# Optimization experiments

Measured on AMD Instinct MI355X. Metric: run time of the kernel, lower is better.

## Reference

```python
import jax, jax.numpy as jnp
import numpy as np

N = 100000   # nodes
E = 3200000  # edges (avg degree 32)
D_IN = 128
C = 64
EPS = 1e-5  # GraphNorm eps (PyG default)


def _graph_norm(x, alpha, gamma, beta):
    # GraphNorm over a single graph: all N nodes form one segment.
    mean = jnp.mean(x, axis=0, keepdims=True)            # [1, C]
    xc = x - alpha * mean                                # learnable mean-scale
    var = jnp.mean(xc * xc, axis=0, keepdims=True)       # [1, C]
    return gamma * xc * jax.lax.rsqrt(var + EPS) + beta


def _gcn_conv(x, W, bias, src, dst, dinv):
    # GCN with implicit self-loops: out = D^-1/2 (A+I) D^-1/2 (x W) + b
    xw = x @ W                                           # [N, C]
    coef = (dinv[src] * dinv[dst])[:, None]              # [E, 1]
    msg = xw[src] * coef                                 # [E, C] gather
    agg = jax.ops.segment_sum(msg, dst, num_segments=N)  # [N, C] scatter
    agg = agg + xw * (dinv * dinv)[:, None]              # self-loop term
    return agg + bias


def setup_inputs() -> dict:
    key = jax.random.key(0)
    ks = jax.random.split(key, 4)
    x = jax.random.normal(ks[0], (N, D_IN), dtype=jnp.float32)
    edge_index = jax.random.randint(ks[1], (2, E), 0, N, dtype=jnp.int64)
    W0 = jax.random.normal(ks[2], (D_IN, C), dtype=jnp.float32) * (1.0 / np.sqrt(D_IN))
    Ws = jax.random.normal(ks[3], (2, C, C), dtype=jnp.float32) * (1.0 / np.sqrt(C))
    b = jnp.zeros((3, C), dtype=jnp.float32)
    alpha = jnp.ones((3, C), dtype=jnp.float32)
    gamma = jnp.ones((3, C), dtype=jnp.float32)
    beta = jnp.zeros((3, C), dtype=jnp.float32)
    return {"x": x, "edge_index": edge_index, "W0": W0, "Ws": Ws,
            "b": b, "alpha": alpha, "gamma": gamma, "beta": beta}


def reference(x, edge_index, W0, Ws, b, alpha, gamma, beta):
    src, dst = edge_index[0], edge_index[1]
    deg = 1.0 + jax.ops.segment_sum(jnp.ones((E,), dtype=x.dtype), dst, num_segments=N)
    dinv = jax.lax.rsqrt(deg)                            # [N]
    h = _gcn_conv(x, W0, b[0], src, dst, dinv)
    h = _graph_norm(h, alpha[0], gamma[0], beta[0])      # dropout = identity (eval)
    for i in range(2):
        h = _gcn_conv(h, Ws[i], b[i + 1], src, dst, dinv)
        h = _graph_norm(h, alpha[i + 1], gamma[i + 1], beta[i + 1])
    return h
```

## Files before the change

### kernel.cpp

```cpp
#include <hip/hip_runtime.h>
#include <hip/hip_bf16.h>


#define EPS 1e-5f

typedef __attribute__((ext_vector_type(8))) short bf16x8;
typedef __attribute__((ext_vector_type(4))) float f32x4;

__device__ __forceinline__ float bf_lo(unsigned u) {
    union { unsigned u; float f; } c; c.u = u << 16; return c.f;
}
__device__ __forceinline__ float bf_hi(unsigned u) {
    union { unsigned u; float f; } c; c.u = u & 0xffff0000u; return c.f;
}
__device__ __forceinline__ unsigned pack_bf2(float a, float b) {
    union { __hip_bfloat16 h; unsigned short u; } ca, cb;
    ca.h = __float2bfloat16(a);
    cb.h = __float2bfloat16(b);
    return (unsigned)ca.u | ((unsigned)cb.u << 16);
}
__device__ __forceinline__ short bfb(float f) {
    union { __hip_bfloat16 h; short s; } u; u.h = __float2bfloat16(f); return u.s;
}

__global__ __launch_bounds__(256) void k_hist(const int* __restrict__ dst, int* __restrict__ hist,
                                              int E, int SEG, int NBKT) {
    __shared__ int h[2048];
    int t = threadIdx.x;
    for (int b = t; b < NBKT; b += 256) h[b] = 0;
    __syncthreads();
    int i0 = blockIdx.x * SEG, i1 = min(E, i0 + SEG);
    for (int i = i0 + t * 4; i < i1; i += 1024) {
        if (i + 3 < i1) {
            int4 d = *(const int4*)(dst + i);
            atomicAdd(&h[d.x >> 6], 1);
            atomicAdd(&h[d.y >> 6], 1);
            atomicAdd(&h[d.z >> 6], 1);
            atomicAdd(&h[d.w >> 6], 1);
        } else {
            for (int q = i; q < i1; ++q) atomicAdd(&h[dst[q] >> 6], 1);
        }
    }
    __syncthreads();
    for (int b = t; b < NBKT; b += 256) hist[blockIdx.x * NBKT + b] = h[b];
}

__global__ __launch_bounds__(256) void k_scanA(const int* __restrict__ hist, int* __restrict__ chunkScan,
                                               int* __restrict__ chunkTot, int NBKT, int SCAN_N) {
    __shared__ int ls[256];
    int t = threadIdx.x;
    int base = blockIdx.x * 1024 + t * 4;
    int v[4];
#pragma unroll
    for (int j = 0; j < 4; ++j) {
        int l = base + j;
        v[j] = 0;
        if (l < SCAN_N) {
            int blk = l & 255, bkt = l >> 8;
            v[j] = hist[blk * NBKT + bkt];
        }
    }
    int s = v[0] + v[1] + v[2] + v[3];
    ls[t] = s;
    __syncthreads();
    for (int off = 1; off < 256; off <<= 1) {
        int val = (t >= off) ? ls[t - off] : 0;
        __syncthreads();
        ls[t] += val;
        __syncthreads();
    }
    int run = ls[t] - s;
#pragma unroll
    for (int j = 0; j < 4; ++j) {
        chunkScan[base + j] = run;
        run += v[j];
    }
    if (t == 255) chunkTot[blockIdx.x] = ls[255];
}

__global__ void k_scanB(const int* __restrict__ chunkTot, int* __restrict__ chunkBase, int NCH) {
    __shared__ int s[512];
    int t = threadIdx.x;
    s[t] = (t < NCH) ? chunkTot[t] : 0;
    s[t + 256] = (t + 256 < NCH) ? chunkTot[t + 256] : 0;
    __syncthreads();
    for (int off = 1; off < 512; off <<= 1) {
        int a0 = (t >= off) ? s[t - off] : 0;
        int a1 = (t + 256 >= off) ? s[t + 256 - off] : 0;
        __syncthreads();
        s[t] += a0;
        s[t + 256] += a1;
        __syncthreads();
    }
    if (t < NCH) chunkBase[t] = t ? s[t - 1] : 0;
    if (t + 256 < NCH) chunkBase[t + 256] = s[t + 255];
}

__global__ __launch_bounds__(256) void k_scatter_part(const int* __restrict__ src, const int* __restrict__ dst,
                                                      const int* __restrict__ chunkScan,
                                                      const int* __restrict__ chunkBase,
                                                      int* __restrict__ packed, int E, int SEG, int NBKT) {
    __shared__ int cur[2048];
    int blk = blockIdx.x, t = threadIdx.x;
    for (int b = t; b < NBKT; b += 256) {
        int l = b * 256 + blk;
        cur[b] = chunkScan[l] + chunkBase[l >> 10];
    }
    __syncthreads();
    int i0 = blk * SEG, i1 = min(E, i0 + SEG);
    for (int i = i0 + t * 4; i < i1; i += 1024) {
        if (i + 3 < i1) {
            int4 d = *(const int4*)(dst + i);
            int4 s = *(const int4*)(src + i);
            int p;
            p = atomicAdd(&cur[d.x >> 6], 1); packed[p] = (int)(((unsigned)(d.x & 63) << 26) | (unsigned)s.x);
            p = atomicAdd(&cur[d.y >> 6], 1); packed[p] = (int)(((unsigned)(d.y & 63) << 26) | (unsigned)s.y);
            p = atomicAdd(&cur[d.z >> 6], 1); packed[p] = (int)(((unsigned)(d.z & 63) << 26) | (unsigned)s.z);
            p = atomicAdd(&cur[d.w >> 6], 1); packed[p] = (int)(((unsigned)(d.w & 63) << 26) | (unsigned)s.w);
        } else {
            for (int q = i; q < i1; ++q) {
                int dd = dst[q];
                int p = atomicAdd(&cur[dd >> 6], 1);
                packed[p] = (int)(((unsigned)(dd & 63) << 26) | (unsigned)src[q]);
            }
        }
    }
}

__global__ __launch_bounds__(256) void k_ellfill(const int* __restrict__ packed,
                                                 const int* __restrict__ chunkScan,
                                                 const int* __restrict__ chunkBase,
                                                 int* __restrict__ ell, int* __restrict__ cursor,
                                                 float* __restrict__ dinv,
                                                 int CAP, int NBKT, int N, int E) {
    __shared__ int ellLoc[64 * 96];
    __shared__ int cnt[64];
    int bkt = blockIdx.x, t = threadIdx.x;
    if (t < 64) cnt[t] = 0;
    __syncthreads();
    int l0 = bkt * 256;
    int bs = chunkScan[l0] + chunkBase[l0 >> 10];
    int be = E;
    if (bkt + 1 < NBKT) {
        int l1 = (bkt + 1) * 256;
        be = chunkScan[l1] + chunkBase[l1 >> 10];
    }
    for (int i = bs + t; i < be; i += 256) {
        unsigned p = (unsigned)packed[i];
        int s = (int)(p & 0x03FFFFFFu);
        int ld = (int)(p >> 26);
        int slot = atomicAdd(&cnt[ld], 1);
        if (slot < CAP) ellLoc[ld * CAP + slot] = s;
    }
    __syncthreads();
    int lo = bkt << 6;
    int total = 64 * CAP;
    for (int idx = t; idx < total; idx += 256) {
        int ld = idx / CAP;
        int s = idx - ld * CAP;
        if (lo + ld < N && s < min(cnt[ld], CAP))
            ell[(size_t)lo * CAP + idx] = ellLoc[idx];
    }
    if (t < 64 && lo + t < N) {
        int dg = min(cnt[t], CAP);
        cursor[lo + t] = (lo + t) * CAP + dg;
        dinv[lo + t] = rsqrtf(1.0f + (float)cnt[t]);
    }
}

__global__ __launch_bounds__(256) void k_cursor_init(int* cursor, int CAP, int n) {
    int i = blockIdx.x * 256 + threadIdx.x;
    if (i < n) cursor[i] = i * CAP;
}

__global__ __launch_bounds__(256) void k_fill_ell(const int* __restrict__ src, const int* __restrict__ dst,
                                                  int* cursor, int* __restrict__ ell, int E,
                                                  int lo, int hi) {
    int i = (blockIdx.x * 256 + threadIdx.x) * 4;
    if (i + 3 < E) {
        int4 d = *(const int4*)(dst + i);
        int4 s = *(const int4*)(src + i);
        if (d.x >= lo && d.x < hi) ell[atomicAdd(&cursor[d.x], 1)] = s.x;
        if (d.y >= lo && d.y < hi) ell[atomicAdd(&cursor[d.y], 1)] = s.y;
        if (d.z >= lo && d.z < hi) ell[atomicAdd(&cursor[d.z], 1)] = s.z;
        if (d.w >= lo && d.w < hi) ell[atomicAdd(&cursor[d.w], 1)] = s.w;
    } else {
        for (int t = i; t < E; ++t) {
            int d = dst[t];
            if (d >= lo && d < hi) ell[atomicAdd(&cursor[d], 1)] = src[t];
        }
    }
}

__global__ __launch_bounds__(256) void k_deg_dinv(const int* __restrict__ cursor, float* dinv, int CAP, int n) {
    int i = blockIdx.x * 256 + threadIdx.x;
    if (i < n) dinv[i] = rsqrtf(1.0f + (float)(cursor[i] - i * CAP));
}

template <int K, bool AFP32>
__global__ __launch_bounds__(256) void gemm_mfma(const void* __restrict__ in_,
                                                 const unsigned short* __restrict__ Wb,
                                                 const float* __restrict__ bbv,
                                                 const float* __restrict__ dinv,
                                                 __hip_bfloat16* __restrict__ out, int N) {
    constexpr int NC = K / 32;
    int tid = threadIdx.x;
    int lane = tid & 63, w = tid >> 6;
    int r0 = blockIdx.x * 64;
    int col = w * 16 + (lane & 15);
    int kg = lane >> 4;

    bf16x8 bfrag[NC];
#pragma unroll
    for (int kc = 0; kc < NC; ++kc)
        bfrag[kc] = *(const bf16x8*)(Wb + (size_t)col * K + kc * 32 + kg * 8);
    float bbc = bbv ? bbv[col] : 0.f;

#pragma unroll 1
    for (int rt = 0; rt < 4; ++rt) {
        int arow = r0 + rt * 16 + (lane & 15);
        int arow_c = min(arow, N - 1);
        f32x4 acc = {0.f, 0.f, 0.f, 0.f};
#pragma unroll
        for (int kc = 0; kc < NC; ++kc) {
            bf16x8 afrag;
            if (AFP32) {
                const float* in = (const float*)in_ + (size_t)arow_c * K + kc * 32 + kg * 8;
                float4 lo = *(const float4*)in;
                float4 hi = *(const float4*)(in + 4);
                union { short s[8]; bf16x8 v; } cv;
                cv.s[0] = bfb(lo.x); cv.s[1] = bfb(lo.y); cv.s[2] = bfb(lo.z); cv.s[3] = bfb(lo.w);
                cv.s[4] = bfb(hi.x); cv.s[5] = bfb(hi.y); cv.s[6] = bfb(hi.z); cv.s[7] = bfb(hi.w);
                afrag = cv.v;
            } else {
                const unsigned short* in = (const unsigned short*)in_;
                afrag = *(const bf16x8*)(in + (size_t)arow_c * K + kc * 32 + kg * 8);
            }
            acc = __builtin_amdgcn_mfma_f32_16x16x32_bf16(afrag, bfrag[kc], acc, 0, 0, 0);
        }
#pragma unroll
        for (int j = 0; j < 4; ++j) {
            int row = r0 + rt * 16 + kg * 4 + j;
            if (row < N)
                out[(size_t)row * 64 + col] = __float2bfloat16((acc[j] + bbc) * dinv[row]);
        }
    }
}

__global__ void k_packW0(const float* __restrict__ W0, unsigned short* __restrict__ Wb) {
    int c = threadIdx.x;
    for (int k = 0; k < 128; ++k) Wb[c * 128 + k] = (unsigned short)bfb(W0[k * 64 + c]);
}

template <bool OUT_BF16>
__global__ __launch_bounds__(256, 4) void k_pull(const int* __restrict__ cursor,
                                                 const int* __restrict__ ell,
                                                 const float* __restrict__ dinv,
                                                 const uint4* __restrict__ xwh,
                                                 const float* __restrict__ bias,
                                                 float* __restrict__ aggf,
                                                 __hip_bfloat16* __restrict__ aggh,
                                                 float* __restrict__ sums, float* __restrict__ sumsq,
                                                 int CAP, int N) {
    int tid = threadIdx.x;
    int lane = tid & 63;
    int g = lane >> 3;
    int cl = lane & 7;
    float bs[8];
#pragma unroll
    for (int k = 0; k < 8; ++k) bs[k] = bias[cl * 8 + k];
    float s_acc[8] = {0, 0, 0, 0, 0, 0, 0, 0};
    float q_acc[8] = {0, 0, 0, 0, 0, 0, 0, 0};

    int slot = (blockIdx.x * 4 + (tid >> 6)) * 8 + g;
    int nslots = gridDim.x * 32;
    for (int n = slot; n < N; n += nslots) {
        int beg = n * CAP, end = cursor[n];
        int last = end - 1;
        float acc[8];
        {
            uint4 v = xwh[(size_t)n * 8 + cl];
            acc[0] = bf_lo(v.x); acc[1] = bf_hi(v.x);
            acc[2] = bf_lo(v.y); acc[3] = bf_hi(v.y);
            acc[4] = bf_lo(v.z); acc[5] = bf_hi(v.z);
            acc[6] = bf_lo(v.w); acc[7] = bf_hi(v.w);
        }
        int i = beg;
        for (; i + 8 <= end; i += 8) {
            int4 ia = *(const int4*)&ell[i];
            int4 ib = *(const int4*)&ell[i + 4];
            uint4 vv[8];
            vv[0] = xwh[(size_t)ia.x * 8 + cl];
            vv[1] = xwh[(size_t)ia.y * 8 + cl];
            vv[2] = xwh[(size_t)ia.z * 8 + cl];
            vv[3] = xwh[(size_t)ia.w * 8 + cl];
            vv[4] = xwh[(size_t)ib.x * 8 + cl];
            vv[5] = xwh[(size_t)ib.y * 8 + cl];
            vv[6] = xwh[(size_t)ib.z * 8 + cl];
            vv[7] = xwh[(size_t)ib.w * 8 + cl];
#pragma unroll
            for (int k = 0; k < 8; ++k) {
                acc[0] += bf_lo(vv[k].x); acc[1] += bf_hi(vv[k].x);
                acc[2] += bf_lo(vv[k].y); acc[3] += bf_hi(vv[k].y);
                acc[4] += bf_lo(vv[k].z); acc[5] += bf_hi(vv[k].z);
                acc[6] += bf_lo(vv[k].w); acc[7] += bf_hi(vv[k].w);
            }
        }
        if (i < end) {
            int4 ia = *(const int4*)&ell[i];
            int4 ib = *(const int4*)&ell[i + 4];
            int ss[8];
            ss[0] = ia.x; ss[1] = ia.y; ss[2] = ia.z; ss[3] = ia.w;
            ss[4] = ib.x; ss[5] = ib.y; ss[6] = ib.z; ss[7] = ib.w;
#pragma unroll
            for (int k = 0; k < 8; ++k) ss[k] = (i + k <= last) ? ss[k] : 0;
            uint4 vv[8];
#pragma unroll
            for (int k = 0; k < 8; ++k) vv[k] = xwh[(size_t)ss[k] * 8 + cl];
#pragma unroll
            for (int k = 0; k < 8; ++k) {
                if (i + k > last) { vv[k].x = 0; vv[k].y = 0; vv[k].z = 0; vv[k].w = 0; }
                acc[0] += bf_lo(vv[k].x); acc[1] += bf_hi(vv[k].x);
                acc[2] += bf_lo(vv[k].y); acc[3] += bf_hi(vv[k].y);
                acc[4] += bf_lo(vv[k].z); acc[5] += bf_hi(vv[k].z);
                acc[6] += bf_lo(vv[k].w); acc[7] += bf_hi(vv[k].w);
            }
        }
        float dn = dinv[n];
        float r[8];
#pragma unroll
        for (int k = 0; k < 8; ++k) {
            r[k] = dn * acc[k] + bs[k];
            s_acc[k] += r[k];
            q_acc[k] += r[k] * r[k];
        }
        if (OUT_BF16) {
            uint4 o;
            o.x = pack_bf2(r[0], r[1]);
            o.y = pack_bf2(r[2], r[3]);
            o.z = pack_bf2(r[4], r[5]);
            o.w = pack_bf2(r[6], r[7]);
            *(uint4*)((unsigned short*)aggh + (size_t)n * 64 + cl * 8) = o;
        } else {
            float4* d4 = (float4*)(aggf + (size_t)n * 64 + cl * 8);
            d4[0] = make_float4(r[0], r[1], r[2], r[3]);
            d4[1] = make_float4(r[4], r[5], r[6], r[7]);
        }
    }

    __shared__ float lsum[256][9], lsq[256][9];
#pragma unroll
    for (int k = 0; k < 8; ++k) { lsum[tid][k] = s_acc[k]; lsq[tid][k] = q_acc[k]; }
    __syncthreads();
    if (tid < 64) {
        int cl_t = tid >> 3, k_t = tid & 7;
        float s = 0.f, q = 0.f;
        for (int j = 0; j < 32; ++j) {
            int l = cl_t + 8 * j;
            s += lsum[l][k_t];
            q += lsq[l][k_t];
        }
        atomicAdd(&sums[tid], s);
        atomicAdd(&sumsq[tid], q);
    }
}

__global__ void k_params2(float* __restrict__ sums, float* __restrict__ sumsq,
                          const float* __restrict__ alpha, const float* __restrict__ gamma,
                          const float* __restrict__ beta, const float* __restrict__ W,
                          float* __restrict__ scale, float* __restrict__ shift,
                          unsigned short* __restrict__ Wb, float* __restrict__ bb, int N) {
    __shared__ float ssc[64], ssh[64];
    int c = threadIdx.x;
    float invN = 1.0f / (float)N;
    float m = sums[c] * invN;
    float ex2 = sumsq[c] * invN;
    float a = alpha[c];
    float var = ex2 - 2.0f * a * m * m + a * a * m * m;
    float sc = gamma[c] * rsqrtf(var + EPS);
    float sh = beta[c] - sc * a * m;
    scale[c] = sc;
    shift[c] = sh;
    ssc[c] = sc;
    ssh[c] = sh;
    sums[c] = 0.f;
    sumsq[c] = 0.f;
    __syncthreads();
    if (W) {
        float acc = 0.f;
        for (int k = 0; k < 64; ++k) {
            float w = W[k * 64 + c];
            Wb[c * 64 + k] = (unsigned short)bfb(ssc[k] * w);
            acc += ssh[k] * w;
        }
        bb[c] = acc;
    }
}

__global__ __launch_bounds__(256) void k_final(float* __restrict__ out, const float* __restrict__ scale,
                                               const float* __restrict__ shift, int n64) {
    int i = blockIdx.x * 256 + threadIdx.x;
    if (i < n64) out[i] = scale[i & 63] * out[i] + shift[i & 63];
}

extern "C" void kernel_launch(void* const* d_in, const int* in_sizes, int n_in,
                              void* d_out, int out_size, void* d_ws, size_t ws_size,
                              hipStream_t stream) {
    const float* x     = (const float*)d_in[0];
    const int*   ei    = (const int*)d_in[1];
    const float* W0    = (const float*)d_in[2];
    const float* Wsp   = (const float*)d_in[3];
    const float* b     = (const float*)d_in[4];
    const float* alpha = (const float*)d_in[5];
    const float* gamma = (const float*)d_in[6];
    const float* beta  = (const float*)d_in[7];

    const int N = in_sizes[0] / 128;
    const int E = in_sizes[1] / 2;
    const int* src = ei;
    const int* dst = ei + E;

    float* aggf = (float*)d_out;

    const int Na = ((N + 63) / 64) * 64;
    float* ws = (float*)d_ws;
    size_t off = 0;
    float* dinv  = ws + off; off += Na;
    __hip_bfloat16* xwh = (__hip_bfloat16*)(ws + off); off += (size_t)Na * 32;
    __hip_bfloat16* hb  = (__hip_bfloat16*)(ws + off); off += (size_t)Na * 32;
    float* sums  = ws + off; off += 64;
    float* sumsq = ws + off; off += 64;
    float* scbuf = ws + off; off += 64;
    float* shbuf = ws + off; off += 64;
    unsigned short* Wb = (unsigned short*)(ws + off); off += 4096;
    float* bbv   = ws + off; off += 64;
    int* cursor  = (int*)(ws + off); off += Na;

    int CAP = 96;
    while (CAP > 72 && (off + (size_t)N * CAP + 8) * 4 > ws_size) CAP -= 8;
    int* ell = (int*)(ws + off); off += (size_t)N * CAP + 8;

    const int n64 = N * 64;
    const int RB = (N + 63) / 64;
    const int NB = (N + 255) / 256;
    const int PB = (N + 63) / 64;

    const int NBKT = (N + 63) >> 6;
    const int NSEG = 256;
    int SEG = ((E + NSEG - 1) / NSEG + 3) & ~3;
    const int SCAN_N = NBKT * 256;
    const int NCH = (SCAN_N + 1023) / 1024;
    int* packed    = (int*)xwh;
    int* hist      = (int*)hb;
    int* chunkScan = hist + (size_t)NSEG * NBKT;
    int* chunkTot  = chunkScan + (size_t)NCH * 1024;
    int* chunkBase = chunkTot + NCH;
    bool fast_build = (NBKT <= 2048) && (NCH <= 512) && (N < (1 << 26)) &&
                      ((size_t)E <= (size_t)Na * 32) &&
                      ((size_t)NSEG * NBKT + (size_t)NCH * 1024 + 2 * NCH <= (size_t)Na * 32);

    if (fast_build) {
        k_hist<<<NSEG, 256, 0, stream>>>(dst, hist, E, SEG, NBKT);
        k_scanA<<<NCH, 256, 0, stream>>>(hist, chunkScan, chunkTot, NBKT, SCAN_N);
        k_scanB<<<1, 256, 0, stream>>>(chunkTot, chunkBase, NCH);
        k_scatter_part<<<NSEG, 256, 0, stream>>>(src, dst, chunkScan, chunkBase, packed, E, SEG, NBKT);
        k_ellfill<<<NBKT, 256, 0, stream>>>(packed, chunkScan, chunkBase, ell, cursor, dinv,
                                            CAP, NBKT, N, E);
    } else {
        k_cursor_init<<<NB, 256, 0, stream>>>(cursor, CAP, N);
        const int NCHUNK = 10;
        int cs = (N + NCHUNK - 1) / NCHUNK;
        const int EB4 = (E / 4 + 255) / 256;
        for (int c = 0; c < NCHUNK; ++c) {
            int lo = c * cs, hi = min(N, lo + cs);
            k_fill_ell<<<EB4, 256, 0, stream>>>(src, dst, cursor, ell, E, lo, hi);
        }
        k_deg_dinv<<<NB, 256, 0, stream>>>(cursor, dinv, CAP, N);
    }

    hipMemsetAsync(sums, 0, 128 * sizeof(float), stream);
    k_packW0<<<1, 64, 0, stream>>>(W0, Wb);

    for (int layer = 0; layer < 3; ++layer) {
        if (layer == 0) {
            gemm_mfma<128, true><<<RB, 256, 0, stream>>>(x, Wb, nullptr, dinv, xwh, N);
        } else {
            gemm_mfma<64, false><<<RB, 256, 0, stream>>>(hb, Wb, bbv, dinv, xwh, N);
        }
        if (layer < 2) {
            k_pull<true><<<PB, 256, 0, stream>>>(cursor, ell, dinv, (const uint4*)xwh,
                                                 b + layer * 64, nullptr, hb,
                                                 sums, sumsq, CAP, N);
        } else {
            k_pull<false><<<PB, 256, 0, stream>>>(cursor, ell, dinv, (const uint4*)xwh,
                                                  b + layer * 64, aggf, nullptr,
                                                  sums, sumsq, CAP, N);
        }
        const float* Wnext = (layer < 2) ? (Wsp + (size_t)layer * 64 * 64) : nullptr;
        k_params2<<<1, 64, 0, stream>>>(sums, sumsq, alpha + layer * 64, gamma + layer * 64,
                                        beta + layer * 64, Wnext, scbuf, shbuf, Wb, bbv, N);
    }
    k_final<<<(n64 + 255) / 256, 256, 0, stream>>>(aggf, scbuf, shbuf, n64);
}
```

Measured before the change: 386.3 us.

## Split feature tables into four 16-channel planes and pull each plane separately

The GEMM now writes its bf16 output as four planar 16-column slabs of 32 bytes per row instead of one 128-byte row. The pull kernel makes four passes, one per slab, gathering 4 bytes per lane from a table four times smaller, so the gathered working set is more likely to stay in cache. The cost is four passes over the ELL index list and cursors, narrower gathers of 32 bytes per neighbor, and more passes' worth of loop overhead.

```diff
diff --git a/kernel.cpp b/kernel.cpp
--- a/kernel.cpp
+++ b/kernel.cpp
@@ -202,7 +202,8 @@
                                                  const unsigned short* __restrict__ Wb,
                                                  const float* __restrict__ bbv,
                                                  const float* __restrict__ dinv,
-                                                 __hip_bfloat16* __restrict__ out, int N) {
+                                                 unsigned short* __restrict__ out16,
+                                                 int N) {
     constexpr int NC = K / 32;
     int tid = threadIdx.x;
     int lane = tid & 63, w = tid >> 6;
@@ -234,7 +235,8 @@
                 afrag = cv.v;
             } else {
                 const unsigned short* in = (const unsigned short*)in_;
-                afrag = *(const bf16x8*)(in + (size_t)arow_c * K + kc * 32 + kg * 8);
+                int pa = kc * 2 + (kg >> 1);
+                afrag = *(const bf16x8*)(in + ((size_t)pa * N + arow_c) * 16 + (kg & 1) * 8);
             }
             acc = __builtin_amdgcn_mfma_f32_16x16x32_bf16(afrag, bfrag[kc], acc, 0, 0, 0);
         }
@@ -242,7 +244,8 @@
         for (int j = 0; j < 4; ++j) {
             int row = r0 + rt * 16 + kg * 4 + j;
             if (row < N)
-                out[(size_t)row * 64 + col] = __float2bfloat16((acc[j] + bbc) * dinv[row]);
+                out16[((size_t)w * N + row) * 16 + (lane & 15)] =
+                    (unsigned short)bfb((acc[j] + bbc) * dinv[row]);
         }
     }
 }
@@ -256,109 +259,90 @@
 __global__ __launch_bounds__(256, 4) void k_pull(const int* __restrict__ cursor,
                                                  const int* __restrict__ ell,
                                                  const float* __restrict__ dinv,
-                                                 const uint4* __restrict__ xwh,
+                                                 const unsigned* __restrict__ xws8,
                                                  const float* __restrict__ bias,
                                                  float* __restrict__ aggf,
-                                                 __hip_bfloat16* __restrict__ aggh,
+                                                 unsigned* __restrict__ aggh8,
                                                  float* __restrict__ sums, float* __restrict__ sumsq,
                                                  int CAP, int N) {
     int tid = threadIdx.x;
     int lane = tid & 63;
     int g = lane >> 3;
     int cl = lane & 7;
-    float bs[8];
-#pragma unroll
-    for (int k = 0; k < 8; ++k) bs[k] = bias[cl * 8 + k];
-    float s_acc[8] = {0, 0, 0, 0, 0, 0, 0, 0};
-    float q_acc[8] = {0, 0, 0, 0, 0, 0, 0, 0};
-
-    int slot = (blockIdx.x * 4 + (tid >> 6)) * 8 + g;
+    __shared__ float lsum[256][9], lsq[256][9];
+
+    int slot0 = (blockIdx.x * 4 + (tid >> 6)) * 8 + g;
     int nslots = gridDim.x * 32;
-    for (int n = slot; n < N; n += nslots) {
-        int beg = n * CAP, end = cursor[n];
-        int last = end - 1;
-        float acc[8];
-        {
-            uint4 v = xwh[(size_t)n * 8 + cl];
-            acc[0] = bf_lo(v.x); acc[1] = bf_hi(v.x);
-            acc[2] = bf_lo(v.y); acc[3] = bf_hi(v.y);
-            acc[4] = bf_lo(v.z); acc[5] = bf_hi(v.z);
-            acc[6] = bf_lo(v.w); acc[7] = bf_hi(v.w);
-        }
-        int i = beg;
-        for (; i + 8 <= end; i += 8) {
-            int4 ia = *(const int4*)&ell[i];
-            int4 ib = *(const int4*)&ell[i + 4];
-            uint4 vv[8];
-            vv[0] = xwh[(size_t)ia.x * 8 + cl];
-            vv[1] = xwh[(size_t)ia.y * 8 + cl];
-            vv[2] = xwh[(size_t)ia.z * 8 + cl];
-            vv[3] = xwh[(size_t)ia.w * 8 + cl];
-            vv[4] = xwh[(size_t)ib.x * 8 + cl];
-            vv[5] = xwh[(size_t)ib.y * 8 + cl];
-            vv[6] = xwh[(size_t)ib.z * 8 + cl];
-            vv[7] = xwh[(size_t)ib.w * 8 + cl];
-#pragma unroll
-            for (int k = 0; k < 8; ++k) {
-                acc[0] += bf_lo(vv[k].x); acc[1] += bf_hi(vv[k].x);
-                acc[2] += bf_lo(vv[k].y); acc[3] += bf_hi(vv[k].y);
-                acc[4] += bf_lo(vv[k].z); acc[5] += bf_hi(vv[k].z);
-                acc[6] += bf_lo(vv[k].w); acc[7] += bf_hi(vv[k].w);
+
+#pragma unroll 1
+    for (int p = 0; p < 4; ++p) {
+        const unsigned* tab = xws8 + (size_t)p * N * 8;
+        float bs0 = bias[p * 16 + cl * 2];
+        float bs1 = bias[p * 16 + cl * 2 + 1];
+        float sp0 = 0.f, sp1 = 0.f, qp0 = 0.f, qp1 = 0.f;
+        for (int n = slot0; n < N; n += nslots) {
+            int beg = n * CAP, end = cursor[n];
+            int last = end - 1;
+            unsigned su = tab[(size_t)n * 8 + cl];
+            float a0 = bf_lo(su), a1 = bf_hi(su);
+            int i = beg;
+            for (; i + 8 <= end; i += 8) {
+                int4 ia = *(const int4*)&ell[i];
+                int4 ib = *(const int4*)&ell[i + 4];
+                unsigned v0 = tab[(size_t)ia.x * 8 + cl];
+                unsigned v1 = tab[(size_t)ia.y * 8 + cl];
+                unsigned v2 = tab[(size_t)ia.z * 8 + cl];
+                unsigned v3 = tab[(size_t)ia.w * 8 + cl];
+                unsigned v4 = tab[(size_t)ib.x * 8 + cl];
+                unsigned v5 = tab[(size_t)ib.y * 8 + cl];
+                unsigned v6 = tab[(size_t)ib.z * 8 + cl];
+                unsigned v7 = tab[(size_t)ib.w * 8 + cl];
+                a0 += bf_lo(v0) + bf_lo(v1) + bf_lo(v2) + bf_lo(v3)
+                    + bf_lo(v4) + bf_lo(v5) + bf_lo(v6) + bf_lo(v7);
+                a1 += bf_hi(v0) + bf_hi(v1) + bf_hi(v2) + bf_hi(v3)
+                    + bf_hi(v4) + bf_hi(v5) + bf_hi(v6) + bf_hi(v7);
             }
-        }
-        if (i < end) {
-            int4 ia = *(const int4*)&ell[i];
-            int4 ib = *(const int4*)&ell[i + 4];
-            int ss[8];
-            ss[0] = ia.x; ss[1] = ia.y; ss[2] = ia.z; ss[3] = ia.w;
-            ss[4] = ib.x; ss[5] = ib.y; ss[6] = ib.z; ss[7] = ib.w;
-#pragma unroll
-            for (int k = 0; k < 8; ++k) ss[k] = (i + k <= last) ? ss[k] : 0;
-            uint4 vv[8];
-#pragma unroll
-            for (int k = 0; k < 8; ++k) vv[k] = xwh[(size_t)ss[k] * 8 + cl];
-#pragma unroll
-            for (int k = 0; k < 8; ++k) {
-                if (i + k > last) { vv[k].x = 0; vv[k].y = 0; vv[k].z = 0; vv[k].w = 0; }
-                acc[0] += bf_lo(vv[k].x); acc[1] += bf_hi(vv[k].x);
-                acc[2] += bf_lo(vv[k].y); acc[3] += bf_hi(vv[k].y);
-                acc[4] += bf_lo(vv[k].z); acc[5] += bf_hi(vv[k].z);
-                acc[6] += bf_lo(vv[k].w); acc[7] += bf_hi(vv[k].w);
+            if (i < end) {
+                int4 ia = *(const int4*)&ell[i];
+                int4 ib = *(const int4*)&ell[i + 4];
+                int ss[8];
+                ss[0] = ia.x; ss[1] = ia.y; ss[2] = ia.z; ss[3] = ia.w;
+                ss[4] = ib.x; ss[5] = ib.y; ss[6] = ib.z; ss[7] = ib.w;
+#pragma unroll
+                for (int k = 0; k < 8; ++k) ss[k] = (i + k <= last) ? ss[k] : 0;
+                unsigned vv[8];
+#pragma unroll
+                for (int k = 0; k < 8; ++k) vv[k] = tab[(size_t)ss[k] * 8 + cl];
+#pragma unroll
+                for (int k = 0; k < 8; ++k) {
+                    if (i + k > last) vv[k] = 0;
+                    a0 += bf_lo(vv[k]);
+                    a1 += bf_hi(vv[k]);
+                }
             }
-        }
-        float dn = dinv[n];
-        float r[8];
-#pragma unroll
-        for (int k = 0; k < 8; ++k) {
-            r[k] = dn * acc[k] + bs[k];
-            s_acc[k] += r[k];
-            q_acc[k] += r[k] * r[k];
-        }
-        if (OUT_BF16) {
-            uint4 o;
-            o.x = pack_bf2(r[0], r[1]);
-            o.y = pack_bf2(r[2], r[3]);
-            o.z = pack_bf2(r[4], r[5]);
-            o.w = pack_bf2(r[6], r[7]);
-            *(uint4*)((unsigned short*)aggh + (size_t)n * 64 + cl * 8) = o;
-        } else {
-            float4* d4 = (float4*)(aggf + (size_t)n * 64 + cl * 8);
-            d4[0] = make_float4(r[0], r[1], r[2], r[3]);
-            d4[1] = make_float4(r[4], r[5], r[6], r[7]);
-        }
-    }
-
-    __shared__ float lsum[256][9], lsq[256][9];
-#pragma unroll
-    for (int k = 0; k < 8; ++k) { lsum[tid][k] = s_acc[k]; lsq[tid][k] = q_acc[k]; }
+            float dn = dinv[n];
+            float r0 = dn * a0 + bs0;
+            float r1 = dn * a1 + bs1;
+            sp0 += r0; qp0 += r0 * r0;
+            sp1 += r1; qp1 += r1 * r1;
+            if (OUT_BF16) {
+                aggh8[(size_t)p * N * 8 + (size_t)n * 8 + cl] = pack_bf2(r0, r1);
+            } else {
+                *(float2*)(aggf + (size_t)n * 64 + p * 16 + cl * 2) = make_float2(r0, r1);
+            }
+        }
+        lsum[tid][p * 2] = sp0;   lsq[tid][p * 2] = qp0;
+        lsum[tid][p * 2 + 1] = sp1; lsq[tid][p * 2 + 1] = qp1;
+    }
     __syncthreads();
     if (tid < 64) {
-        int cl_t = tid >> 3, k_t = tid & 7;
+        int p = tid >> 4, rem = tid & 15, cl_t = rem >> 1, bq = rem & 1;
+        int k = p * 2 + bq;
         float s = 0.f, q = 0.f;
         for (int j = 0; j < 32; ++j) {
             int l = cl_t + 8 * j;
-            s += lsum[l][k_t];
-            q += lsq[l][k_t];
+            s += lsum[l][k];
+            q += lsq[l][k];
         }
         atomicAdd(&sums[tid], s);
         atomicAdd(&sumsq[tid], q);
@@ -426,8 +410,8 @@
     float* ws = (float*)d_ws;
     size_t off = 0;
     float* dinv  = ws + off; off += Na;
-    __hip_bfloat16* xwh = (__hip_bfloat16*)(ws + off); off += (size_t)Na * 32;
-    __hip_bfloat16* hb  = (__hip_bfloat16*)(ws + off); off += (size_t)Na * 32;
+    unsigned short* xws = (unsigned short*)(ws + off); off += (size_t)Na * 32;
+    unsigned short* hbs = (unsigned short*)(ws + off); off += (size_t)Na * 32;
     float* sums  = ws + off; off += 64;
     float* sumsq = ws + off; off += 64;
     float* scbuf = ws + off; off += 64;
@@ -450,8 +434,8 @@
     int SEG = ((E + NSEG - 1) / NSEG + 3) & ~3;
     const int SCAN_N = NBKT * 256;
     const int NCH = (SCAN_N + 1023) / 1024;
-    int* packed    = (int*)xwh;
-    int* hist      = (int*)hb;
+    int* packed    = (int*)xws;
+    int* hist      = (int*)hbs;
     int* chunkScan = hist + (size_t)NSEG * NBKT;
     int* chunkTot  = chunkScan + (size_t)NCH * 1024;
     int* chunkBase = chunkTot + NCH;
@@ -483,16 +467,16 @@
 
     for (int layer = 0; layer < 3; ++layer) {
         if (layer == 0) {
-            gemm_mfma<128, true><<<RB, 256, 0, stream>>>(x, Wb, nullptr, dinv, xwh, N);
+            gemm_mfma<128, true><<<RB, 256, 0, stream>>>(x, Wb, nullptr, dinv, xws, N);
         } else {
-            gemm_mfma<64, false><<<RB, 256, 0, stream>>>(hb, Wb, bbv, dinv, xwh, N);
+            gemm_mfma<64, false><<<RB, 256, 0, stream>>>(hbs, Wb, bbv, dinv, xws, N);
         }
         if (layer < 2) {
-            k_pull<true><<<PB, 256, 0, stream>>>(cursor, ell, dinv, (const uint4*)xwh,
-                                                 b + layer * 64, nullptr, hb,
+            k_pull<true><<<PB, 256, 0, stream>>>(cursor, ell, dinv, (const unsigned*)xws,
+                                                 b + layer * 64, nullptr, (unsigned*)hbs,
                                                  sums, sumsq, CAP, N);
         } else {
-            k_pull<false><<<PB, 256, 0, stream>>>(cursor, ell, dinv, (const uint4*)xwh,
+            k_pull<false><<<PB, 256, 0, stream>>>(cursor, ell, dinv, (const unsigned*)xws,
                                                   b + layer * 64, aggf, nullptr,
                                                   sums, sumsq, CAP, N);
         }
```

After: 579.0 us. 49.9% more time.
